# Optimization experiments

Hardware: AMD Instinct MI355X
Metric: run time of the kernel (lower is better)

## Reference

```python
import jax, jax.numpy as jnp
import numpy as np

NUM_HEADS = 16
NUM_GROUPS = 32  # min(C//4, 32) with C=1024
EPS = 1e-6       # flax GroupNorm default


def setup_inputs() -> dict:
    key = jax.random.key(0)
    ks = jax.random.split(key, 3)
    B, L, C = 2, 2048, 1024
    x = jax.random.normal(ks[0], (B, L, C), dtype=jnp.float32)
    gn_scale = jnp.ones((C,), jnp.float32)
    gn_bias = jnp.zeros((C,), jnp.float32)
    qkv_w = jax.random.normal(ks[1], (C, 3 * C), jnp.float32) * (C ** -0.5)
    qkv_b = jnp.zeros((3 * C,), jnp.float32)
    proj_w = jax.random.normal(ks[2], (C, C), jnp.float32) * 1e-5  # default_init(1e-10) ~ tiny
    proj_b = jnp.zeros((C,), jnp.float32)
    return {"x": x, "gn_scale": gn_scale, "gn_bias": gn_bias,
            "qkv_w": qkv_w, "qkv_b": qkv_b, "proj_w": proj_w, "proj_b": proj_b}


def reference(x, gn_scale, gn_bias, qkv_w, qkv_b, proj_w, proj_b):
    B, L, C = x.shape
    H = NUM_HEADS
    hd = C // H
    # GroupNorm over (L, channels-in-group)
    xg = x.reshape(B, L, NUM_GROUPS, C // NUM_GROUPS)
    mu = jnp.mean(xg, axis=(1, 3), keepdims=True)
    var = jnp.var(xg, axis=(1, 3), keepdims=True)
    xn = ((xg - mu) * jax.lax.rsqrt(var + EPS)).reshape(B, L, C)
    xn = xn * gn_scale + gn_bias
    # 1x1-conv QKV projection == dense
    qkv = xn @ qkv_w + qkv_b                       # [B, L, 3C]
    qkv = qkv.reshape(B, L, H, 3 * hd)             # interleaved per-head q|k|v
    q, k, v = jnp.split(qkv, 3, axis=-1)           # each [B, L, H, hd]
    scale = 1.0 / jnp.sqrt(hd)
    logits = jnp.einsum('btnh,bfnh->bnft', k, q * scale)  # [B, H, L, L]
    weights = jax.nn.softmax(logits, axis=-1)
    h = jnp.einsum('bnft,btnh->bfnh', weights, v).reshape(B, L, C)
    h = h @ proj_w + proj_b
    # CombineResidualSkip, project_skip=False
    return (x + h) / np.sqrt(2.0)
```

## Files before the change

### kernel.cpp

```cpp
#include <hip/hip_runtime.h>
#include <hip/hip_bf16.h>

typedef __hip_bfloat16 bf16;
typedef __attribute__((ext_vector_type(8))) __bf16 bf16x8;
typedef __attribute__((ext_vector_type(4))) float floatx4;

#define NB 2
#define NL 2048
#define NC 1024
#define NH 16
#define ND 64

__device__ __forceinline__ void async_copy16(void* lds, const void* g) {
  __builtin_amdgcn_global_load_lds(
      (__attribute__((address_space(1))) void*)(const_cast<void*>(g)),
      (__attribute__((address_space(3))) void*)(lds), 16, 0, 0);
}

__device__ __forceinline__ floatx4 mfma16(bf16x8 a, bf16x8 b, floatx4 c) {
  return __builtin_amdgcn_mfma_f32_16x16x32_bf16(a, b, c, 0, 0, 0);
}

__global__ __launch_bounds__(256) void gn_part_kernel(
    const float* __restrict__ x, float2* __restrict__ part) {
  int bg = blockIdx.x >> 3, sl = blockIdx.x & 7;
  int b = bg >> 5, g = bg & 31;
  const float* base = x + (size_t)b * NL * NC + (size_t)(sl * 256) * NC + g * 32;
  float s = 0.f, ss = 0.f;
  for (int vi = threadIdx.x; vi < 2048; vi += 256) {
    int l = vi >> 3, j = (vi & 7) * 4;
    float4 u = *(const float4*)(base + (size_t)l * NC + j);
    s += u.x + u.y + u.z + u.w;
    ss += u.x * u.x + u.y * u.y + u.z * u.z + u.w * u.w;
  }
  for (int off = 32; off; off >>= 1) {
    s += __shfl_down(s, off);
    ss += __shfl_down(ss, off);
  }
  __shared__ float rs[4], rss[4];
  int wave = threadIdx.x >> 6, lane = threadIdx.x & 63;
  if (lane == 0) { rs[wave] = s; rss[wave] = ss; }
  __syncthreads();
  if (threadIdx.x == 0) {
    part[blockIdx.x] = make_float2(rs[0] + rs[1] + rs[2] + rs[3],
                                   rss[0] + rss[1] + rss[2] + rss[3]);
  }
}

__global__ __launch_bounds__(256) void gn_apply_kernel(
    const float* __restrict__ x, const float2* __restrict__ part,
    const float* __restrict__ scale, const float* __restrict__ bias,
    bf16* __restrict__ xn) {
  size_t idx = (size_t)blockIdx.x * 256 + threadIdx.x;
  size_t e = idx * 8;
  int c = (int)(e & (NC - 1));
  int b = (int)(e >> 21);
  int bg = b * 32 + (c >> 5);
  float s = 0.f, ss = 0.f;
#pragma unroll
  for (int i = 0; i < 8; ++i) {
    float2 p = part[bg * 8 + i];
    s += p.x; ss += p.y;
  }
  float mean = s * (1.f / 65536.f);
  float var = ss * (1.f / 65536.f) - mean * mean;
  float rstd = rsqrtf(var + 1e-6f);
  float4 x0 = *(const float4*)(x + e);
  float4 x1 = *(const float4*)(x + e + 4);
  float4 s0 = *(const float4*)(scale + c);
  float4 s1 = *(const float4*)(scale + c + 4);
  float4 b0 = *(const float4*)(bias + c);
  float4 b1 = *(const float4*)(bias + c + 4);
  float xv[8] = {x0.x, x0.y, x0.z, x0.w, x1.x, x1.y, x1.z, x1.w};
  float sv[8] = {s0.x, s0.y, s0.z, s0.w, s1.x, s1.y, s1.z, s1.w};
  float bv[8] = {b0.x, b0.y, b0.z, b0.w, b1.x, b1.y, b1.z, b1.w};
  bf16 o[8];
#pragma unroll
  for (int k = 0; k < 8; ++k)
    o[k] = __float2bfloat16((xv[k] - mean) * rstd * sv[k] + bv[k]);
  *(uint4*)(xn + e) = *(const uint4*)o;
}

__global__ void transpose_f32_bf16(const float* __restrict__ in,
                                   bf16* __restrict__ out, int R, int C) {
  __shared__ float t[32][33];
  int c0 = blockIdx.x * 32, r0 = blockIdx.y * 32;
#pragma unroll
  for (int j = 0; j < 4; ++j)
    t[threadIdx.y + j * 8][threadIdx.x] =
        in[(size_t)(r0 + threadIdx.y + j * 8) * C + c0 + threadIdx.x];
  __syncthreads();
#pragma unroll
  for (int j = 0; j < 4; ++j)
    out[(size_t)(c0 + threadIdx.y + j * 8) * R + r0 + threadIdx.x] =
        __float2bfloat16(t[threadIdx.x][threadIdx.y + j * 8]);
}

template <int MODE, int NT>
__global__ __launch_bounds__(256) void gemm_kernel(
    const bf16* __restrict__ A, const bf16* __restrict__ Bt,
    const float* __restrict__ biasv, const float* __restrict__ xres,
    bf16* __restrict__ Qo, bf16* __restrict__ Ko, bf16* __restrict__ Vto,
    float* __restrict__ out, int M, int N, int K) {
  constexpr int NFR = NT / 32;
  __shared__ bf16 As[128 * 32];
  __shared__ bf16 Bs[NT * 32];
  int tid = threadIdx.x, wave = tid >> 6, lane = tid & 63;
  int col = lane & 15, quad = lane >> 4;
  int mB = blockIdx.y * 128, nB = blockIdx.x * NT;
  int wm = (wave >> 1) * 64, wn = (wave & 1) * (NT / 2);
  floatx4 acc[4][NFR];
#pragma unroll
  for (int i = 0; i < 4; ++i)
#pragma unroll
    for (int j = 0; j < NFR; ++j) acc[i][j] = (floatx4){0.f, 0.f, 0.f, 0.f};

  int rowOff = wave * 32 + (lane >> 2);
  int rowOffB = (NT == 128) ? rowOff : (wave * 16 + (lane >> 2));
  int kOff = (lane & 3) * 8;

  for (int k0 = 0; k0 < K; k0 += 32) {
    __syncthreads();
    const bf16* ga = A + (size_t)(mB + rowOff) * K + k0 + kOff;
    async_copy16(&As[(wave * 32) * 32], ga);
    async_copy16(&As[(wave * 32 + 16) * 32], ga + (size_t)16 * K);
    const bf16* gb = Bt + (size_t)(nB + rowOffB) * K + k0 + kOff;
    if (NT == 128) {
      async_copy16(&Bs[(wave * 32) * 32], gb);
      async_copy16(&Bs[(wave * 32 + 16) * 32], gb + (size_t)16 * K);
    } else {
      async_copy16(&Bs[(wave * 16) * 32], gb);
    }
    __syncthreads();
    bf16x8 af[4], bfr[NFR];
#pragma unroll
    for (int mi = 0; mi < 4; ++mi)
      af[mi] = *(const bf16x8*)&As[(wm + mi * 16 + col) * 32 + quad * 8];
#pragma unroll
    for (int ni = 0; ni < NFR; ++ni)
      bfr[ni] = *(const bf16x8*)&Bs[(wn + ni * 16 + col) * 32 + quad * 8];
#pragma unroll
    for (int mi = 0; mi < 4; ++mi)
#pragma unroll
      for (int ni = 0; ni < NFR; ++ni)
        acc[mi][ni] = mfma16(af[mi], bfr[ni], acc[mi][ni]);
  }

#pragma unroll
  for (int mi = 0; mi < 4; ++mi)
#pragma unroll
    for (int ni = 0; ni < NFR; ++ni)
#pragma unroll
      for (int r = 0; r < 4; ++r) {
        int row = mB + wm + mi * 16 + quad * 4 + r;
        int ncol = nB + wn + ni * 16 + col;
        float v = acc[mi][ni][r] + biasv[ncol];
        if (MODE == 0) {
          int b = row >> 11, f = row & 2047;
          int h = ncol / 192, rr = ncol - h * 192;
          size_t bhl = ((size_t)(b * NH + h) * NL + f);
          if (rr < 64)
            Qo[bhl * 64 + rr] = __float2bfloat16(v * 0.125f);
          else if (rr < 128)
            Ko[bhl * 64 + rr - 64] = __float2bfloat16(v);
          else
            Vto[((size_t)(b * NH + h) * 64 + (rr - 128)) * NL + f] = __float2bfloat16(v);
        } else {
          size_t o = (size_t)row * N + ncol;
          out[o] = (xres[o] + v) * 0.70710678118654752f;
        }
      }
}

__global__ __launch_bounds__(512, 2) void attn_kernel(
    const bf16* __restrict__ Q, const bf16* __restrict__ Kb,
    const bf16* __restrict__ Vt, bf16* __restrict__ hout) {
  int qt = blockIdx.x, bh = blockIdx.y;
  int b = bh >> 4, h = bh & 15;
  int tid = threadIdx.x, wave = tid >> 6, lane = tid & 63;
  int m = lane & 15, quad = lane >> 4;

  __shared__ bf16 Kd[2][4096];
  __shared__ bf16 Vd[2][4096];
  __shared__ bf16 Pp[8][2048];

  bf16* Psw = Pp[wave];

  const bf16* Kg = Kb + (size_t)bh * NL * 64;
  const bf16* Vg = Vt + (size_t)bh * 64 * NL;

  bf16x8 bq[2][2];
  {
    const bf16* Qg = Q + ((size_t)bh * NL + qt * 256 + wave * 32) * 64;
#pragma unroll
    for (int nf = 0; nf < 2; ++nf)
#pragma unroll
      for (int c = 0; c < 2; ++c)
        bq[nf][c] = *(const bf16x8*)&Qg[(size_t)(nf * 16 + m) * 64 + c * 32 + quad * 8];
  }

  float lrow[2] = {0.f, 0.f};
  floatx4 o[2][4];
#pragma unroll
  for (int nf = 0; nf < 2; ++nf)
#pragma unroll
    for (int di = 0; di < 4; ++di) o[nf][di] = (floatx4){0.f, 0.f, 0.f, 0.f};

  int srow = lane >> 3, schunk = lane & 7;

  auto stage = [&](int bufi, int t0) {
    int r0 = wave * 8;
    int r = r0 + srow;
    int cg = schunk ^ (r & 7);
    async_copy16(&Kd[bufi][r0 * 64], Kg + (size_t)(t0 + r) * 64 + cg * 8);
    async_copy16(&Vd[bufi][r0 * 64], Vg + (size_t)r * NL + t0 + cg * 8);
  };

  stage(0, 0);
  __syncthreads();

  int buf = 0;
  for (int t0 = 0; t0 < NL; t0 += 64) {
    if (t0 + 64 < NL) stage(buf ^ 1, t0 + 64);

    const bf16* Kbase = Kd[buf];
    const bf16* Vbase = Vd[buf];

    floatx4 s[2][4];
#pragma unroll
    for (int nf = 0; nf < 2; ++nf)
#pragma unroll
      for (int ti = 0; ti < 4; ++ti) s[nf][ti] = (floatx4){0.f, 0.f, 0.f, 0.f};
#pragma unroll
    for (int ti = 0; ti < 4; ++ti)
#pragma unroll
      for (int c = 0; c < 2; ++c) {
        bf16x8 ak = *(const bf16x8*)
            &Kbase[(ti * 16 + m) * 64 + ((c * 4 + quad) ^ (m & 7)) * 8];
        s[0][ti] = mfma16(ak, bq[0][c], s[0][ti]);
        s[1][ti] = mfma16(ak, bq[1][c], s[1][ti]);
      }

#pragma unroll
    for (int nf = 0; nf < 2; ++nf) {
      float ls = 0.f;
#pragma unroll
      for (int ti = 0; ti < 4; ++ti)
#pragma unroll
        for (int r = 0; r < 4; ++r) {
          float p = __expf(s[nf][ti][r]);
          s[nf][ti][r] = p;
          ls += p;
        }
      ls += __shfl_xor(ls, 16);
      ls += __shfl_xor(ls, 32);
      lrow[nf] += ls;
#pragma unroll
      for (int ti = 0; ti < 4; ++ti) {
        bf16 pk[4];
#pragma unroll
        for (int r = 0; r < 4; ++r) pk[r] = __float2bfloat16(s[nf][ti][r]);
        int ct = ti * 2 + (quad >> 1);
        *(uint2*)&Psw[(nf * 16 + m) * 64 + ((ct ^ (m & 7)) * 8) + (quad & 1) * 4] =
            *(const uint2*)pk;
      }
    }

#pragma unroll
    for (int c = 0; c < 2; ++c) {
      bf16x8 bp[2];
#pragma unroll
      for (int nf = 0; nf < 2; ++nf)
        bp[nf] = *(const bf16x8*)
            &Psw[(nf * 16 + m) * 64 + (((c * 4 + quad) ^ (m & 7)) * 8)];
#pragma unroll
      for (int di = 0; di < 4; ++di) {
        bf16x8 av = *(const bf16x8*)
            &Vbase[(di * 16 + m) * 64 + ((c * 4 + quad) ^ (m & 7)) * 8];
        o[0][di] = mfma16(av, bp[0], o[0][di]);
        o[1][di] = mfma16(av, bp[1], o[1][di]);
      }
    }

    __syncthreads();
    buf ^= 1;
  }

#pragma unroll
  for (int nf = 0; nf < 2; ++nf) {
    float rl = 1.f / lrow[nf];
    int l = qt * 256 + wave * 32 + nf * 16 + m;
    bf16* hp = hout + (size_t)(b * NL + l) * NC + h * 64;
#pragma unroll
    for (int di = 0; di < 4; ++di) {
      bf16 pk[4];
#pragma unroll
      for (int r = 0; r < 4; ++r) pk[r] = __float2bfloat16(o[nf][di][r] * rl);
      *(uint2*)&hp[di * 16 + quad * 4] = *(const uint2*)pk;
    }
  }
}

extern "C" void kernel_launch(void* const* d_in, const int* in_sizes, int n_in,
                              void* d_out, int out_size, void* d_ws, size_t ws_size,
                              hipStream_t stream) {
  const float* x = (const float*)d_in[0];
  const float* gn_scale = (const float*)d_in[1];
  const float* gn_bias = (const float*)d_in[2];
  const float* qkv_w = (const float*)d_in[3];
  const float* qkv_b = (const float*)d_in[4];
  const float* proj_w = (const float*)d_in[5];
  const float* proj_b = (const float*)d_in[6];
  float* out = (float*)d_out;

  bf16* xn = (bf16*)d_out;

  char* ws = (char*)d_ws;
  float2* part = (float2*)ws;
  bf16* Qb = (bf16*)(ws + 4096);
  bf16* Kbuf = Qb + 4194304;
  bf16* Vt = Kbuf + 4194304;
  bf16* hat = Vt + 4194304;
  bf16* wqkvT = hat;
  bf16* projT = Qb;

  gn_part_kernel<<<512, 256, 0, stream>>>(x, part);
  gn_apply_kernel<<<2048, 256, 0, stream>>>(x, part, gn_scale, gn_bias, xn);
  transpose_f32_bf16<<<dim3(96, 32), dim3(32, 8), 0, stream>>>(qkv_w, wqkvT, 1024, 3072);
  gemm_kernel<0, 128><<<dim3(24, 32), 256, 0, stream>>>(
      xn, wqkvT, qkv_b, nullptr, Qb, Kbuf, Vt, nullptr, 4096, 3072, 1024);
  attn_kernel<<<dim3(8, 32), 512, 0, stream>>>(Qb, Kbuf, Vt, hat);
  transpose_f32_bf16<<<dim3(32, 32), dim3(32, 8), 0, stream>>>(proj_w, projT, 1024, 1024);
  gemm_kernel<1, 64><<<dim3(16, 32), 256, 0, stream>>>(
      hat, projT, proj_b, x, nullptr, nullptr, nullptr, out, 4096, 1024, 1024);
}
```

Baseline: 218.2 us.

## Fuse GN stats with QKV weight transpose, vectorize V store, use exp2 softmax

Merges the GroupNorm partial-sum kernel with the QKV weight transpose into one launch to save a kernel launch. The QKV epilogue now writes V^T as packed 4-element stores and folds log2(e) into the Q scale so the softmax can use exp2f. Attention is split into two launches over halves of the batch-head dimension. This may reduce per-launch occupancy, since each launch now has fewer blocks.

```diff
diff --git a/kernel.cpp b/kernel.cpp
--- a/kernel.cpp
+++ b/kernel.cpp
@@ -21,29 +21,47 @@
   return __builtin_amdgcn_mfma_f32_16x16x32_bf16(a, b, c, 0, 0, 0);
 }
 
-__global__ __launch_bounds__(256) void gn_part_kernel(
-    const float* __restrict__ x, float2* __restrict__ part) {
-  int bg = blockIdx.x >> 3, sl = blockIdx.x & 7;
-  int b = bg >> 5, g = bg & 31;
-  const float* base = x + (size_t)b * NL * NC + (size_t)(sl * 256) * NC + g * 32;
-  float s = 0.f, ss = 0.f;
-  for (int vi = threadIdx.x; vi < 2048; vi += 256) {
-    int l = vi >> 3, j = (vi & 7) * 4;
-    float4 u = *(const float4*)(base + (size_t)l * NC + j);
-    s += u.x + u.y + u.z + u.w;
-    ss += u.x * u.x + u.y * u.y + u.z * u.z + u.w * u.w;
-  }
-  for (int off = 32; off; off >>= 1) {
-    s += __shfl_down(s, off);
-    ss += __shfl_down(ss, off);
-  }
+__global__ __launch_bounds__(256) void prep_kernel(
+    const float* __restrict__ x, float2* __restrict__ part,
+    const float* __restrict__ qkv_w, bf16* __restrict__ wqkvT) {
+  __shared__ float t[32][33];
   __shared__ float rs[4], rss[4];
-  int wave = threadIdx.x >> 6, lane = threadIdx.x & 63;
-  if (lane == 0) { rs[wave] = s; rss[wave] = ss; }
-  __syncthreads();
-  if (threadIdx.x == 0) {
-    part[blockIdx.x] = make_float2(rs[0] + rs[1] + rs[2] + rs[3],
-                                   rss[0] + rss[1] + rss[2] + rss[3]);
+  int tid = threadIdx.x;
+  if (blockIdx.x < 512) {
+    int bg = blockIdx.x >> 3, sl = blockIdx.x & 7;
+    int b = bg >> 5, g = bg & 31;
+    const float* base = x + (size_t)b * NL * NC + (size_t)(sl * 256) * NC + g * 32;
+    float s = 0.f, ss = 0.f;
+    for (int vi = tid; vi < 2048; vi += 256) {
+      int l = vi >> 3, j = (vi & 7) * 4;
+      float4 u = *(const float4*)(base + (size_t)l * NC + j);
+      s += u.x + u.y + u.z + u.w;
+      ss += u.x * u.x + u.y * u.y + u.z * u.z + u.w * u.w;
+    }
+    for (int off = 32; off; off >>= 1) {
+      s += __shfl_down(s, off);
+      ss += __shfl_down(ss, off);
+    }
+    int wave = tid >> 6, lane = tid & 63;
+    if (lane == 0) { rs[wave] = s; rss[wave] = ss; }
+    __syncthreads();
+    if (tid == 0) {
+      part[blockIdx.x] = make_float2(rs[0] + rs[1] + rs[2] + rs[3],
+                                     rss[0] + rss[1] + rss[2] + rss[3]);
+    }
+  } else {
+    int tb = blockIdx.x - 512;
+    int bx = tb % 96, by = tb / 96;
+    int tx = tid & 31, ty = tid >> 5;
+    int c0 = bx * 32, r0 = by * 32;
+#pragma unroll
+    for (int j = 0; j < 4; ++j)
+      t[ty + j * 8][tx] = qkv_w[(size_t)(r0 + ty + j * 8) * 3072 + c0 + tx];
+    __syncthreads();
+#pragma unroll
+    for (int j = 0; j < 4; ++j)
+      wqkvT[(size_t)(c0 + ty + j * 8) * 1024 + r0 + tx] =
+          __float2bfloat16(t[tx][ty + j * 8]);
   }
 }
 
@@ -149,33 +167,45 @@
 #pragma unroll
   for (int mi = 0; mi < 4; ++mi)
 #pragma unroll
-    for (int ni = 0; ni < NFR; ++ni)
-#pragma unroll
-      for (int r = 0; r < 4; ++r) {
-        int row = mB + wm + mi * 16 + quad * 4 + r;
-        int ncol = nB + wn + ni * 16 + col;
-        float v = acc[mi][ni][r] + biasv[ncol];
-        if (MODE == 0) {
-          int b = row >> 11, f = row & 2047;
-          int h = ncol / 192, rr = ncol - h * 192;
-          size_t bhl = ((size_t)(b * NH + h) * NL + f);
-          if (rr < 64)
-            Qo[bhl * 64 + rr] = __float2bfloat16(v * 0.125f);
-          else if (rr < 128)
-            Ko[bhl * 64 + rr - 64] = __float2bfloat16(v);
-          else
-            Vto[((size_t)(b * NH + h) * 64 + (rr - 128)) * NL + f] = __float2bfloat16(v);
+    for (int ni = 0; ni < NFR; ++ni) {
+      int row0 = mB + wm + mi * 16 + quad * 4;
+      int ncol = nB + wn + ni * 16 + col;
+      float vv[4];
+#pragma unroll
+      for (int r = 0; r < 4; ++r) vv[r] = acc[mi][ni][r] + biasv[ncol];
+      if (MODE == 0) {
+        int b = row0 >> 11, f0 = row0 & 2047;
+        int h = ncol / 192, rr = ncol - h * 192;
+        size_t bh = (size_t)(b * NH + h);
+        if (rr < 64) {
+#pragma unroll
+          for (int r = 0; r < 4; ++r)
+            Qo[(bh * NL + f0 + r) * 64 + rr] =
+                __float2bfloat16(vv[r] * 0.18033688011112042f);
+        } else if (rr < 128) {
+#pragma unroll
+          for (int r = 0; r < 4; ++r)
+            Ko[(bh * NL + f0 + r) * 64 + rr - 64] = __float2bfloat16(vv[r]);
         } else {
-          size_t o = (size_t)row * N + ncol;
-          out[o] = (xres[o] + v) * 0.70710678118654752f;
+          bf16 pk[4];
+#pragma unroll
+          for (int r = 0; r < 4; ++r) pk[r] = __float2bfloat16(vv[r]);
+          *(uint2*)&Vto[(bh * 64 + (rr - 128)) * NL + f0] = *(const uint2*)pk;
+        }
+      } else {
+#pragma unroll
+        for (int r = 0; r < 4; ++r) {
+          size_t o = (size_t)(row0 + r) * N + ncol;
+          out[o] = (xres[o] + vv[r]) * 0.70710678118654752f;
         }
       }
+    }
 }
 
 __global__ __launch_bounds__(512, 2) void attn_kernel(
     const bf16* __restrict__ Q, const bf16* __restrict__ Kb,
-    const bf16* __restrict__ Vt, bf16* __restrict__ hout) {
-  int qt = blockIdx.x, bh = blockIdx.y;
+    const bf16* __restrict__ Vt, bf16* __restrict__ hout, int byoff) {
+  int qt = blockIdx.x, bh = blockIdx.y + byoff;
   int b = bh >> 4, h = bh & 15;
   int tid = threadIdx.x, wave = tid >> 6, lane = tid & 63;
   int m = lane & 15, quad = lane >> 4;
@@ -248,7 +278,7 @@
       for (int ti = 0; ti < 4; ++ti)
 #pragma unroll
         for (int r = 0; r < 4; ++r) {
-          float p = __expf(s[nf][ti][r]);
+          float p = exp2f(s[nf][ti][r]);
           s[nf][ti][r] = p;
           ls += p;
         }
@@ -324,12 +354,12 @@
   bf16* wqkvT = hat;
   bf16* projT = Qb;
 
-  gn_part_kernel<<<512, 256, 0, stream>>>(x, part);
+  prep_kernel<<<3584, 256, 0, stream>>>(x, part, qkv_w, wqkvT);
   gn_apply_kernel<<<2048, 256, 0, stream>>>(x, part, gn_scale, gn_bias, xn);
-  transpose_f32_bf16<<<dim3(96, 32), dim3(32, 8), 0, stream>>>(qkv_w, wqkvT, 1024, 3072);
   gemm_kernel<0, 128><<<dim3(24, 32), 256, 0, stream>>>(
       xn, wqkvT, qkv_b, nullptr, Qb, Kbuf, Vt, nullptr, 4096, 3072, 1024);
-  attn_kernel<<<dim3(8, 32), 512, 0, stream>>>(Qb, Kbuf, Vt, hat);
+  attn_kernel<<<dim3(8, 16), 512, 0, stream>>>(Qb, Kbuf, Vt, hat, 0);
+  attn_kernel<<<dim3(8, 16), 512, 0, stream>>>(Qb, Kbuf, Vt, hat, 16);
   transpose_f32_bf16<<<dim3(32, 32), dim3(32, 8), 0, stream>>>(proj_w, projT, 1024, 1024);
   gemm_kernel<1, 64><<<dim3(16, 32), 256, 0, stream>>>(
       hat, projT, proj_b, x, nullptr, nullptr, nullptr, out, 4096, 1024, 1024);
```

Measured after the change: 286.2 us. +31.2%, slower.
